# Performance work log

Hardware: AMD Instinct MI355X
Metric: run time of the kernel (lower is better)

Reference implementation:

```python
import jax, jax.numpy as jnp
import numpy as np
from jax import lax

NUM_THRESH = 100  # torch.linspace(0, 1, steps=100)


def _neighbor_max(lab):
    # 4-connectivity neighbor max with zero padding; lab: [T, B, H, W] int32
    up = jnp.pad(lab[:, :, 1:, :], ((0, 0), (0, 0), (0, 1), (0, 0)))
    dn = jnp.pad(lab[:, :, :-1, :], ((0, 0), (0, 0), (1, 0), (0, 0)))
    lf = jnp.pad(lab[:, :, :, 1:], ((0, 0), (0, 0), (0, 0), (0, 1)))
    rt = jnp.pad(lab[:, :, :, :-1], ((0, 0), (0, 0), (0, 0), (1, 0)))
    return jnp.maximum(jnp.maximum(up, dn), jnp.maximum(lf, rt))


def count_components(binz):
    # binz: [T, B, H, W] float {0,1}. Parallel CCL via iterative max-label
    # propagation (the vectorized equivalent of the source's per-pixel DFS).
    T, B, H, W = binz.shape
    ids = (jnp.arange(H * W, dtype=jnp.int32) + 1).reshape(H, W)  # unique id per pixel
    mask = binz > 0
    lab0 = jnp.where(mask, ids, 0).astype(jnp.int32)

    def body(_, lab):
        return jnp.where(mask, jnp.maximum(lab, _neighbor_max(lab)), 0)

    lab = lax.fori_loop(0, 2 * (H + W), body, lab0)
    # one representative pixel per component keeps its own id (the max id)
    roots = jnp.logical_and(lab == ids, mask)
    return jnp.sum(roots.astype(jnp.float32), axis=(2, 3))  # [T, B]


def euler_number(binz):
    # euler = #pixels - #4-connected edges  (faithful to compute_euler_number)
    px = jnp.sum(binz, axis=(2, 3))
    ev = jnp.sum(binz[:, :, :-1, :] * binz[:, :, 1:, :], axis=(2, 3))
    eh = jnp.sum(binz[:, :, :, :-1] * binz[:, :, :, 1:], axis=(2, 3))
    return px - (ev + eh)  # [T, B]


def compute_betti_numbers(prob, thresholds):
    # prob: [B, H, W] -> betti: [B, T, 2] with (b0, b1), b1 = b0 - euler
    binz = (prob[None] > thresholds[:, None, None, None]).astype(jnp.float32)
    b0 = count_components(binz)          # [T, B]
    b1 = b0 - euler_number(binz)          # [T, B]
    return jnp.stack([b0, b1], axis=-1).transpose(1, 0, 2)  # [B, T, 2]


def setup_inputs() -> dict:
    key = jax.random.key(0)
    k1, k2 = jax.random.split(key)
    three_class_prob = jax.random.uniform(k1, (8, 3, 64, 64), dtype=jnp.float32)
    gt_betti = jax.random.randint(k2, (8, 3, NUM_THRESH, 2), 0, 10, dtype=jnp.int32)
    return {"three_class_prob": three_class_prob, "gt_betti": gt_betti}


def reference(three_class_prob, gt_betti):
    thresholds = jnp.linspace(0.0, 1.0, NUM_THRESH, dtype=jnp.float32)
    inside_betti = compute_betti_numbers(three_class_prob[:, 0], thresholds)
    boundary_betti = compute_betti_numbers(three_class_prob[:, 1], thresholds)
    union_betti = inside_betti  # source uses channel 0 slice for 'union' too
    gt = gt_betti.astype(jnp.float32)
    err = (jnp.sum(jnp.abs(inside_betti - gt[:, 0]), axis=(1, 2))
           + jnp.sum(jnp.abs(boundary_betti - gt[:, 1]), axis=(1, 2))
           + jnp.sum(jnp.abs(union_betti - gt[:, 2]), axis=(1, 2)))
    return err  # [B] per-image topology error
```

## Files before the change

kernel.cpp:

```cpp
#include <hip/hip_runtime.h>

typedef unsigned long long ull;
#define NT 100

__device__ __forceinline__ int find_root(int* P, int x) {
    int p = P[x];
    while (p != x) {
        int gp = P[p];
        P[x] = gp;
        x = gp;
        p = P[x];
    }
    return x;
}

__device__ __forceinline__ int unite(int* P, int a, int b) {
    a = find_root(P, a);
    b = find_root(P, b);
    while (a != b) {
        if (a < b) { int t = a; a = b; b = t; }
        int old = atomicCAS(&P[a], a, b);
        if (old == a) return 1;
        a = find_root(P, old);
        b = find_root(P, b);
    }
    return 0;
}

__global__ __launch_bounds__(256)
void betti_partial(const float* __restrict__ prob,
                   ull* __restrict__ ws)
{
    __shared__ int P[2048];
    __shared__ int bL[3][64];
    __shared__ int bR[3][64];

    const int d    = blockIdx.x;
    const int tile = (d & 7) * 200 + (d >> 3);
    const int t    = tile % NT;
    const int cb   = tile / NT;

    const float thr = (float)t * (1.0f / 99.0f);
    const float* img = prob + (size_t)((cb >> 1) * 3 + (cb & 1)) * 4096;

    const int tid  = threadIdx.x;
    const int h    = tid >> 6;
    const int lane = tid & 63;

    const float4* rp = (const float4*)(img + (lane << 6) + (h << 4));
    unsigned int m = 0;
    #pragma unroll
    for (int q = 0; q < 4; ++q) {
        float4 v = rp[q];
        m |= (unsigned)(v.x > thr) << (4 * q + 0);
        m |= (unsigned)(v.y > thr) << (4 * q + 1);
        m |= (unsigned)(v.z > thr) << (4 * q + 2);
        m |= (unsigned)(v.w > thr) << (4 * q + 3);
    }

    #pragma unroll
    for (int k = 0; k < 8; ++k) {
        int s = ((h * 8 + k) << 6) | lane;
        P[s] = s;
    }

    const unsigned um = m & 0xFFFFu;
    unsigned up        = (unsigned)__shfl_up((int)um, 1, 64);
    unsigned starts    = um & ~(um << 1) & 0xFFFFu;
    unsigned starts_up = (unsigned)__shfl_up((int)starts, 1, 64);
    if (lane == 0) { up = 0u; starts_up = 0u; }

    const int px    = __popc(um);
    int       eh    = __popc(um & (um >> 1));
    const int ev    = __popc(um & up);
    const int nruns = __popc(starts);

    if (h < 3)
        bL[h][lane] = ((um >> 15) & 1u) ? (((h * 8 + (nruns - 1)) << 6) | lane) : -1;
    if (h > 0)
        bR[h - 1][lane] = (um & 1u) ? (((h * 8) << 6) | lane) : -1;

    int merges = 0;
    unsigned ov = um & up;
    unsigned ss = ov & ~(ov << 1) & 0xFFFFu;
    while (ss) {
        int j = __ffs(ss) - 1;
        ss &= ss - 1;
        unsigned le = (2u << j) - 1;
        int kc = __popc(starts    & le) - 1;
        int ku = __popc(starts_up & le) - 1;
        merges += unite(P, ((h * 8 + kc) << 6) | lane, ((h * 8 + ku) << 6) | (lane - 1));
    }

    __syncthreads();

    if (h < 3) {
        int l = bL[h][lane], r = bR[h][lane];
        if (l >= 0 && r >= 0) { eh++; merges += unite(P, l, r); }
    }

    ull pk = (ull)px
           | ((ull)eh     << 13)
           | ((ull)ev     << 25)
           | ((ull)nruns  << 37)
           | ((ull)merges << 49);
    #pragma unroll
    for (int o = 32; o > 0; o >>= 1)
        pk += __shfl_down(pk, o, 64);

    if (lane == 0) ws[(size_t)tile * 4 + h] = pk;
}

__global__ __launch_bounds__(256)
void betti_final(const ull* __restrict__ ws,
                 const int* __restrict__ gt,
                 float* __restrict__ out)
{
    __shared__ int wsum[4];
    const int b = blockIdx.x;
    const int tid = threadIdx.x;

    int contrib = 0;
    if (tid < 200) {
        const ull* p = ws + (size_t)(b * 200 + tid) * 4;
        ull s = p[0] + p[1] + p[2] + p[3];
        const int px = (int)( s        & 0x1FFF);
        const int eh = (int)((s >> 13) & 0xFFF);
        const int ev = (int)((s >> 25) & 0xFFF);
        const int nr = (int)((s >> 37) & 0xFFF);
        const int mg = (int)((s >> 49) & 0xFFF);
        const int b0 = nr - mg;
        const int b1 = b0 - (px - (eh + ev));

        const int c = tid / 100;
        const int t = tid - c * 100;
        int d;
        if (c == 0) {
            const int* g0 = gt + (((size_t)b * 3 + 0) * NT + t) * 2;
            const int* g2 = gt + (((size_t)b * 3 + 2) * NT + t) * 2;
            d = b0 - g0[0]; contrib += d < 0 ? -d : d;
            d = b1 - g0[1]; contrib += d < 0 ? -d : d;
            d = b0 - g2[0]; contrib += d < 0 ? -d : d;
            d = b1 - g2[1]; contrib += d < 0 ? -d : d;
        } else {
            const int* g1 = gt + (((size_t)b * 3 + 1) * NT + t) * 2;
            d = b0 - g1[0]; contrib += d < 0 ? -d : d;
            d = b1 - g1[1]; contrib += d < 0 ? -d : d;
        }
    }

    #pragma unroll
    for (int o = 32; o > 0; o >>= 1) contrib += __shfl_down(contrib, o, 64);
    if ((tid & 63) == 0) wsum[tid >> 6] = contrib;
    __syncthreads();
    if (tid == 0)
        out[b] = (float)(wsum[0] + wsum[1] + wsum[2] + wsum[3]);
}

extern "C" void kernel_launch(void* const* d_in, const int* in_sizes, int n_in,
                              void* d_out, int out_size, void* d_ws, size_t ws_size,
                              hipStream_t stream) {
    const float* prob = (const float*)d_in[0];
    const int*   gt   = (const int*)d_in[1];
    float* out = (float*)d_out;
    ull* ws = (ull*)d_ws;

    const int nblocks = 8 * 2 * NT;
    betti_partial<<<nblocks, 256, 0, stream>>>(prob, ws);
    betti_final<<<8, 256, 0, stream>>>(ws, gt, out);
}
```

Baseline: 18.81 us.

## Fuse final reduction into partial kernel via last-block atomic counter

Merges the two kernels into one. Each block bumps a per-batch atomic counter after writing its partials, and the block that completes a batch's 200 tiles runs the final gt comparison and reduction. This removes a second kernel launch and its launch gap. In exchange it adds a device-scope atomic and an extra barrier to every block, and it relies on the counter in the workspace surviving across calls, since the modulo check never resets it.

```diff
diff --git a/kernel.cpp b/kernel.cpp
--- a/kernel.cpp
+++ b/kernel.cpp
@@ -28,20 +28,25 @@
 }
 
 __global__ __launch_bounds__(256)
-void betti_partial(const float* __restrict__ prob,
-                   ull* __restrict__ ws)
+void betti_lastblock(const float* __restrict__ prob,
+                     const int*  __restrict__ gt,
+                     ull* __restrict__ ws,
+                     float* __restrict__ out)
 {
     __shared__ int P[2048];
     __shared__ int bL[3][64];
     __shared__ int bR[3][64];
+    __shared__ int wsum[4];
+    __shared__ int amFin;
 
     const int d    = blockIdx.x;
     const int tile = (d & 7) * 200 + (d >> 3);
     const int t    = tile % NT;
     const int cb   = tile / NT;
+    const int b    = cb >> 1;
 
     const float thr = (float)t * (1.0f / 99.0f);
-    const float* img = prob + (size_t)((cb >> 1) * 3 + (cb & 1)) * 4096;
+    const float* img = prob + (size_t)(b * 3 + (cb & 1)) * 4096;
 
     const int tid  = threadIdx.x;
     const int h    = tid >> 6;
@@ -109,43 +114,43 @@
         pk += __shfl_down(pk, o, 64);
 
     if (lane == 0) ws[(size_t)tile * 4 + h] = pk;
-}
 
-__global__ __launch_bounds__(256)
-void betti_final(const ull* __restrict__ ws,
-                 const int* __restrict__ gt,
-                 float* __restrict__ out)
-{
-    __shared__ int wsum[4];
-    const int b = blockIdx.x;
-    const int tid = threadIdx.x;
+    __syncthreads();
+    if (tid == 0) {
+        ull newv = __hip_atomic_fetch_add(&ws[6400 + (size_t)b * 8], 1ull,
+                                          __ATOMIC_ACQ_REL,
+                                          __HIP_MEMORY_SCOPE_AGENT) + 1ull;
+        amFin = (newv % 200ull == 0ull) ? 1 : 0;
+    }
+    __syncthreads();
+    if (!amFin) return;
 
     int contrib = 0;
     if (tid < 200) {
         const ull* p = ws + (size_t)(b * 200 + tid) * 4;
         ull s = p[0] + p[1] + p[2] + p[3];
-        const int px = (int)( s        & 0x1FFF);
-        const int eh = (int)((s >> 13) & 0xFFF);
-        const int ev = (int)((s >> 25) & 0xFFF);
-        const int nr = (int)((s >> 37) & 0xFFF);
-        const int mg = (int)((s >> 49) & 0xFFF);
-        const int b0 = nr - mg;
-        const int b1 = b0 - (px - (eh + ev));
+        const int spx = (int)( s        & 0x1FFF);
+        const int seh = (int)((s >> 13) & 0xFFF);
+        const int sev = (int)((s >> 25) & 0xFFF);
+        const int nr  = (int)((s >> 37) & 0xFFF);
+        const int mg  = (int)((s >> 49) & 0xFFF);
+        const int b0  = nr - mg;
+        const int b1  = b0 - (spx - (seh + sev));
 
-        const int c = tid / 100;
-        const int t = tid - c * 100;
-        int d;
+        const int c  = tid / 100;
+        const int tt = tid - c * 100;
+        int dd;
         if (c == 0) {
-            const int* g0 = gt + (((size_t)b * 3 + 0) * NT + t) * 2;
-            const int* g2 = gt + (((size_t)b * 3 + 2) * NT + t) * 2;
-            d = b0 - g0[0]; contrib += d < 0 ? -d : d;
-            d = b1 - g0[1]; contrib += d < 0 ? -d : d;
-            d = b0 - g2[0]; contrib += d < 0 ? -d : d;
-            d = b1 - g2[1]; contrib += d < 0 ? -d : d;
+            const int* g0 = gt + (((size_t)b * 3 + 0) * NT + tt) * 2;
+            const int* g2 = gt + (((size_t)b * 3 + 2) * NT + tt) * 2;
+            dd = b0 - g0[0]; contrib += dd < 0 ? -dd : dd;
+            dd = b1 - g0[1]; contrib += dd < 0 ? -dd : dd;
+            dd = b0 - g2[0]; contrib += dd < 0 ? -dd : dd;
+            dd = b1 - g2[1]; contrib += dd < 0 ? -dd : dd;
         } else {
-            const int* g1 = gt + (((size_t)b * 3 + 1) * NT + t) * 2;
-            d = b0 - g1[0]; contrib += d < 0 ? -d : d;
-            d = b1 - g1[1]; contrib += d < 0 ? -d : d;
+            const int* g1 = gt + (((size_t)b * 3 + 1) * NT + tt) * 2;
+            dd = b0 - g1[0]; contrib += dd < 0 ? -dd : dd;
+            dd = b1 - g1[1]; contrib += dd < 0 ? -dd : dd;
         }
     }
 
@@ -166,6 +171,5 @@
     ull* ws = (ull*)d_ws;
 
     const int nblocks = 8 * 2 * NT;
-    betti_partial<<<nblocks, 256, 0, stream>>>(prob, ws);
-    betti_final<<<8, 256, 0, stream>>>(ws, gt, out);
+    betti_lastblock<<<nblocks, 256, 0, stream>>>(prob, gt, ws, out);
 }
```

Measured after the change: 36.81 us. 95.7% more time.
